# Optimization experiments

Hardware: AMD Instinct MI355X
Metric: run time of the kernel (lower is better)

## Reference

```python
import jax, jax.numpy as jnp
import numpy as np

DIM = 768
H = 12
DH = DIM // H          # 64
ROPE_DIM = (DH // 6) * 6   # 60
HALF = (ROPE_DIM // 3) // 2  # 10 freqs per axis
THETA = 10000.0
EPS = 1e-6


def rmsnorm(x, w):
    xf = x.astype(jnp.float32)
    var = jnp.mean(xf * xf, axis=-1, keepdims=True)
    return (w * (xf * jax.lax.rsqrt(var + EPS))).astype(x.dtype)


def rope_angles(positions):
    # positions: [B, N, 3] -> angles [B, N, 3*HALF]
    freqs = 1.0 / (THETA ** (jnp.arange(HALF, dtype=jnp.float32) / HALF))  # [HALF]
    # [B,N,3,1] * [1,1,1,HALF] -> [B,N,3,HALF] -> concat over axis order x,y,z
    ang = positions[..., :, None] * freqs[None, None, None, :]
    return ang.reshape(*positions.shape[:2], 3 * HALF)  # [B,N,30]


def apply_rope(t, cos, sin):
    # t: [B,N,H,ROPE_DIM]; cos/sin: [B,N,1,ROPE_DIM//2]
    B, N, Hh, D = t.shape
    tf = t.astype(jnp.float32).reshape(B, N, Hh, D // 2, 2)
    te, to = tf[..., 0], tf[..., 1]
    oe = te * cos - to * sin
    oo = te * sin + to * cos
    return jnp.stack([oe, oo], axis=-1).reshape(B, N, Hh, D).astype(t.dtype)


def setup_inputs() -> dict:
    key = jax.random.key(0)
    ks = jax.random.split(key, 5)
    B, N = 2, 2048
    x = jax.random.normal(ks[0], (B, N, DIM), dtype=jnp.float32)
    positions = jax.random.uniform(ks[1], (B, N, 3), dtype=jnp.float32)
    qkv_w = jax.random.normal(ks[2], (3 * DIM, DIM), dtype=jnp.float32) * (DIM ** -0.5)
    proj_w = jax.random.normal(ks[3], (DIM, DIM), dtype=jnp.float32) * (DIM ** -0.5)
    proj_b = jnp.zeros((DIM,), dtype=jnp.float32)
    qn_w = jnp.ones((DH,), dtype=jnp.float32)
    kn_w = jnp.ones((DH,), dtype=jnp.float32)
    return {"x": x, "positions": positions, "qkv_w": qkv_w, "proj_w": proj_w,
            "proj_b": proj_b, "qn_w": qn_w, "kn_w": kn_w}


def reference(x, positions, qkv_w, proj_w, proj_b, qn_w, kn_w):
    B, N, C = x.shape
    scale = DH ** -0.5
    qkv = (x @ qkv_w.T).reshape(B, N, 3, H, DH)
    q, k, v = qkv[:, :, 0], qkv[:, :, 1], qkv[:, :, 2]  # [B,N,H,DH]
    q = rmsnorm(q, qn_w)
    k = rmsnorm(k, kn_w)
    # 3D RoPE on first ROPE_DIM channels
    ang = rope_angles(positions)                 # [B,N,30]
    cos = jnp.cos(ang)[:, :, None, :]            # [B,N,1,30]
    sin = jnp.sin(ang)[:, :, None, :]
    q = jnp.concatenate([apply_rope(q[..., :ROPE_DIM], cos, sin), q[..., ROPE_DIM:]], axis=-1)
    k = jnp.concatenate([apply_rope(k[..., :ROPE_DIM], cos, sin), k[..., ROPE_DIM:]], axis=-1)
    attn = jnp.einsum('bqhd,bkhd->bhqk', q, k) * scale  # [B,H,N,N]
    attn = jax.nn.softmax(attn, axis=-1)
    out = jnp.einsum('bhqk,bkhd->bqhd', attn, v).reshape(B, N, C)
    return out @ proj_w.T + proj_b
```

## Files before the change

kernel.cpp:

```cpp
#include <hip/hip_runtime.h>
#include <hip/hip_bf16.h>
#include <math.h>

#define DIM 768
#define NH 12
#define DH 64
#define SEQ 2048
#define BATCH 2
#define TOK (BATCH*SEQ)
#define QKVN (3*DIM)

typedef __attribute__((ext_vector_type(8))) short bf16x8;
typedef __attribute__((ext_vector_type(4))) float f32x4;
typedef __attribute__((ext_vector_type(2))) unsigned int u32x2;
typedef unsigned short u16;

#define VM0 asm volatile("s_waitcnt vmcnt(0)" ::: "memory")
#define VM3 asm volatile("s_waitcnt vmcnt(3)" ::: "memory")
#define VM4 asm volatile("s_waitcnt vmcnt(4)" ::: "memory")
#define LGKM0 asm volatile("s_waitcnt lgkmcnt(0)" ::: "memory")
#define BAR() __builtin_amdgcn_s_barrier()

__device__ inline u16 f2bf(float f) {
  union { float f; unsigned u; } v; v.f = f;
  unsigned u = v.u;
  u += 0x7fffu + ((u >> 16) & 1u);
  return (u16)(u >> 16);
}

__device__ inline int pkbf(float a, float b) {
  __hip_bfloat162 h = __float22bfloat162_rn(make_float2(a, b));
  int r; __builtin_memcpy(&r, &h, 4); return r;
}

__global__ void conv_all(const float* __restrict__ a, u16* __restrict__ ao, int na4,
                         const float* __restrict__ b, u16* __restrict__ bo, int nb4,
                         const float* __restrict__ c, u16* __restrict__ co, int nc4,
                         const float* __restrict__ pos, float2* __restrict__ tab) {
  int i4 = blockIdx.x * blockDim.x + threadIdx.x;
  const int nconv = na4 + nb4 + nc4;
  if (i4 < nconv) {
    const float* src; u16* dst; int off;
    if (i4 < na4)            { src = a; dst = ao; off = i4; }
    else if (i4 < na4 + nb4) { src = b; dst = bo; off = i4 - na4; }
    else                     { src = c; dst = co; off = i4 - na4 - nb4; }
    float4 v = ((const float4*)src)[off];
    ushort4 o;
    o.x = f2bf(v.x); o.y = f2bf(v.y); o.z = f2bf(v.z); o.w = f2bf(v.w);
    ((ushort4*)dst)[off] = o;
    return;
  }
  int e = i4 - nconv;
  if (e >= TOK * 32) return;
  int t = e >> 5, p = e & 31;
  float cs = 1.f, sn = 0.f;
  if (p < 30) {
    int axis = p / 10, fi = p % 10;
    float freq = exp2f(-(float)fi * 1.3287712379549449f);
    float ang = pos[t * 3 + axis] * freq;
    cs = cosf(ang); sn = sinf(ang);
  }
  tab[e] = make_float2(cs, sn);
}

#define GLL(g, s) __builtin_amdgcn_global_load_lds((const __attribute__((address_space(1))) void*)(g), (__attribute__((address_space(3))) void*)(s), 16, 0, 0)

__global__ __launch_bounds__(256, 4) void gemm64(
    const u16* __restrict__ A, const u16* __restrict__ W,
    float* __restrict__ C, const float* __restrict__ bias,
    int M, int Nn, int K)
{
  __shared__ u16 As[2][64 * 64];
  __shared__ u16 Bs[2][64 * 64];
  const int t = threadIdx.x;
  const int w = t >> 6, l = t & 63;
  const int lr = l & 15, lg = l >> 4;
  const int wr = w >> 1, wc = w & 1;
  const int m0 = blockIdx.x * 64;
  const int n0 = blockIdx.y * 64;
  f32x4 acc[2][2] = {};
  const int srow = t >> 3;
  const int scol = (((t & 7) ^ (srow & 7)) * 8);
  const u16* aSrc = A + (size_t)(m0 + srow) * K + scol;
  const u16* bSrc = W + (size_t)(n0 + srow) * K + scol;
  const size_t r32 = (size_t)32 * K;
  const int sw = lr & 7;
  const int NT = K / 64;

  GLL(aSrc,       &As[0][w * 512]);
  GLL(aSrc + r32, &As[0][2048 + w * 512]);
  GLL(bSrc,       &Bs[0][w * 512]);
  GLL(bSrc + r32, &Bs[0][2048 + w * 512]);

  for (int kt = 0; kt < NT; ++kt) {
    const int cur = kt & 1;
    if (kt + 1 < NT) {
      const int k0 = (kt + 1) * 64;
      GLL(aSrc + k0,       &As[cur ^ 1][w * 512]);
      GLL(aSrc + r32 + k0, &As[cur ^ 1][2048 + w * 512]);
      GLL(bSrc + k0,       &Bs[cur ^ 1][w * 512]);
      GLL(bSrc + r32 + k0, &Bs[cur ^ 1][2048 + w * 512]);
      VM4;
    } else {
      VM0;
    }
    BAR();
#pragma unroll
    for (int kk = 0; kk < 2; ++kk) {
      bf16x8 af[2], bff[2];
#pragma unroll
      for (int mi = 0; mi < 2; ++mi)
        af[mi] = *(const bf16x8*)(&As[cur][0] + (wr * 32 + mi * 16 + lr) * 64 + (((kk * 4 + lg) ^ sw) * 8));
#pragma unroll
      for (int ni = 0; ni < 2; ++ni)
        bff[ni] = *(const bf16x8*)(&Bs[cur][0] + (wc * 32 + ni * 16 + lr) * 64 + (((kk * 4 + lg) ^ sw) * 8));
#pragma unroll
      for (int mi = 0; mi < 2; ++mi)
#pragma unroll
        for (int ni = 0; ni < 2; ++ni)
          acc[mi][ni] = __builtin_amdgcn_mfma_f32_16x16x32_bf16(af[mi], bff[ni], acc[mi][ni], 0, 0, 0);
    }
    LGKM0;
    BAR();
  }

#pragma unroll
  for (int mi = 0; mi < 2; ++mi)
#pragma unroll
    for (int ni = 0; ni < 2; ++ni)
#pragma unroll
      for (int r = 0; r < 4; ++r) {
        int row = m0 + wr * 32 + mi * 16 + lg * 4 + r;
        int col = n0 + wc * 32 + ni * 16 + lr;
        C[(size_t)row * Nn + col] = acc[mi][ni][r] + bias[col];
      }
}

__global__ __launch_bounds__(512, 6) void gemm_qkv(
    const u16* __restrict__ A, const u16* __restrict__ W,
    const float* __restrict__ qn_w, const float* __restrict__ kn_w,
    const float2* __restrict__ tab,
    u16* __restrict__ Qb, u16* __restrict__ Kb, u16* __restrict__ Vtb)
{
  __shared__ u16 As[2][128 * 64];
  __shared__ u16 Bs[2][64 * 64];
  const int K = DIM;
  const int t = threadIdx.x;
  const int w = t >> 6, l = t & 63;
  const int lr = l & 15, lg = l >> 4;
  const int m0 = blockIdx.x * 128;
  const int n0 = blockIdx.y * 64;
  f32x4 acc[4] = {};
  const int srow = t >> 3;
  const int scol = (((t & 7) ^ (srow & 7)) * 8);
  const u16* aSrc = A + (size_t)(m0 + srow) * K + scol;
  const u16* bSrc = W + (size_t)(n0 + srow) * K + scol;
  const size_t r64 = (size_t)64 * K;
  const int sw = lr & 7;
  const int NT = K / 64;

  GLL(aSrc,       &As[0][w * 512]);
  GLL(aSrc + r64, &As[0][4096 + w * 512]);
  GLL(bSrc,       &Bs[0][w * 512]);

  for (int kt = 0; kt < NT; ++kt) {
    const int cur = kt & 1;
    if (kt + 1 < NT) {
      const int k0 = (kt + 1) * 64;
      GLL(aSrc + k0,       &As[cur ^ 1][w * 512]);
      GLL(aSrc + r64 + k0, &As[cur ^ 1][4096 + w * 512]);
      GLL(bSrc + k0,       &Bs[cur ^ 1][w * 512]);
      VM3;
    } else {
      VM0;
    }
    BAR();
#pragma unroll
    for (int kk = 0; kk < 2; ++kk) {
      bf16x8 af = *(const bf16x8*)(&As[cur][0] + (w * 16 + lr) * 64 + (((kk * 4 + lg) ^ sw) * 8));
      bf16x8 bff[4];
#pragma unroll
      for (int ni = 0; ni < 4; ++ni)
        bff[ni] = *(const bf16x8*)(&Bs[cur][0] + (ni * 16 + lr) * 64 + (((kk * 4 + lg) ^ sw) * 8));
#pragma unroll
      for (int ni = 0; ni < 4; ++ni)
        acc[ni] = __builtin_amdgcn_mfma_f32_16x16x32_bf16(af, bff[ni], acc[ni], 0, 0, 0);
    }
    LGKM0;
    BAR();
  }

  const int chunk = n0 >> 6;
  const int tt = chunk / 12;
  const int h  = chunk % 12;
  const int bB = m0 >> 11;
  const int bh = bB * NH + h;

  if (tt == 2) {
    const int nbase = (m0 + w * 16 + lg * 4) & 2047;
#pragma unroll
    for (int ni = 0; ni < 4; ++ni) {
      const int d = ni * 16 + lr;
      ushort4 o;
      o.x = f2bf(acc[ni][0]); o.y = f2bf(acc[ni][1]);
      o.z = f2bf(acc[ni][2]); o.w = f2bf(acc[ni][3]);
      *(ushort4*)(Vtb + ((size_t)bh * DH + d) * SEQ + nbase) = o;
    }
  } else {
    const float* wv = (tt == 0 ? qn_w : kn_w);
    const float qs = (tt == 0 ? 0.125f * 1.4426950408889634f : 1.f);
    float wgt[4];
#pragma unroll
    for (int ni = 0; ni < 4; ++ni) wgt[ni] = wv[ni * 16 + lr];
    u16* outp = (tt == 0 ? Qb : Kb) + (size_t)bh * SEQ * DH;
#pragma unroll
    for (int r = 0; r < 4; ++r) {
      float ss = 0.f;
#pragma unroll
      for (int ni = 0; ni < 4; ++ni) ss += acc[ni][r] * acc[ni][r];
      ss += __shfl_xor(ss, 1, 64);
      ss += __shfl_xor(ss, 2, 64);
      ss += __shfl_xor(ss, 4, 64);
      ss += __shfl_xor(ss, 8, 64);
      const float rms = rsqrtf(ss * (1.f / 64.f) + 1e-6f);
      const int trow = m0 + w * 16 + lg * 4 + r;
      const float2* tl = tab + trow * 32;
      u16* rowp = outp + (size_t)(trow & 2047) * DH;
#pragma unroll
      for (int ni = 0; ni < 4; ++ni) {
        const int d = ni * 16 + lr;
        float v = acc[ni][r] * rms * wgt[ni];
        float vp = __shfl_xor(v, 1, 64);
        float2 cssn = tl[ni * 8 + (lr >> 1)];
        float sgn = (d & 1) ? cssn.y : -cssn.y;
        rowp[d] = f2bf((v * cssn.x + vp * sgn) * qs);
      }
    }
  }
}

__global__ __launch_bounds__(256, 3) void attn(
    const u16* __restrict__ Qb, const u16* __restrict__ Kb,
    const u16* __restrict__ Vtb, u16* __restrict__ Ob)
{
  __shared__ u16 Ks[2][2][64 * 64];
  __shared__ u16 Vs[2][64 * 64];
  const int tid = threadIdx.x;
  const int w = tid >> 6, l = tid & 63;
  const int lr = l & 15, lg = l >> 4;
  const int qg = w & 1, half = w >> 1;
  const int wg = blockIdx.x;
  const int swz = (wg & 7) * 96 + (wg >> 3);
  const int bh = swz >> 5;
  const int q0 = (swz & 31) * 64;
  const u16* Qp = Qb + (size_t)bh * SEQ * DH;
  const u16* Kp = Kb + (size_t)bh * SEQ * DH;
  const u16* Vp = Vtb + (size_t)bh * DH * SEQ;

  const int qrA = q0 + qg * 32 + lr;
  const bf16x8 bq0a = *(const bf16x8*)(Qp + (size_t)qrA * DH + 8 * lg);
  const bf16x8 bq1a = *(const bf16x8*)(Qp + (size_t)qrA * DH + 32 + 8 * lg);
  const bf16x8 bq0b = *(const bf16x8*)(Qp + (size_t)(qrA + 16) * DH + 8 * lg);
  const bf16x8 bq1b = *(const bf16x8*)(Qp + (size_t)(qrA + 16) * DH + 32 + 8 * lg);

  const int srow = tid >> 3;
  const int sc16 = (tid & 7) ^ (srow & 7);
  const u16* kSrc = Kp + (size_t)srow * DH + sc16 * 8;
  const u16* vSrc = Vp + (size_t)srow * SEQ + sc16 * 8;

  const int frow = (lr & 3) | ((lr & 4) << 1) | ((lr & 8) >> 1);
  const int ksw = frow & 7;
  const int vsw = lr & 7;

  bf16x8 vone;
#pragma unroll
  for (int j = 0; j < 8; ++j) vone[j] = (short)0x3F80;

  f32x4 oaccA[4] = {}, oaccB[4] = {};
  f32x4 laccA = {}, laccB = {};

  GLL(kSrc,          &Ks[0][0][w * 512]);
  GLL(kSrc + 2048,   &Ks[0][0][w * 512 + 2048]);
  GLL(kSrc + 4096,   &Ks[0][1][w * 512]);
  GLL(kSrc + 6144,   &Ks[0][1][w * 512 + 2048]);
  VM0;
  BAR();
  GLL(vSrc,              &Vs[0][w * 512]);
  GLL(vSrc + 65536,      &Vs[0][w * 512 + 2048]);
  GLL(vSrc + 64,         &Vs[1][w * 512]);
  GLL(vSrc + 64 + 65536, &Vs[1][w * 512 + 2048]);
  GLL(kSrc + 8192,   &Ks[1][0][w * 512]);
  GLL(kSrc + 10240,  &Ks[1][0][w * 512 + 2048]);
  GLL(kSrc + 12288,  &Ks[1][1][w * 512]);
  GLL(kSrc + 14336,  &Ks[1][1][w * 512 + 2048]);

  for (int i = 0; i < 16; ++i) {
    const int p = i & 1;
    const u16* Kt = &Ks[p][half][0];
    const u16* Vt = &Vs[half][0];

    f32x4 paccA[4] = {}, paccB[4] = {};
    __builtin_amdgcn_s_setprio(1);
#pragma unroll
    for (int c = 0; c < 4; ++c) {
      const int rbase = (16 * c + frow) * 64;
      bf16x8 ka = *(const bf16x8*)(Kt + rbase + ((lg ^ ksw) * 8));
      bf16x8 kb = *(const bf16x8*)(Kt + rbase + (((4 + lg) ^ ksw) * 8));
      paccA[c] = __builtin_amdgcn_mfma_f32_16x16x32_bf16(ka, bq0a, paccA[c], 0, 0, 0);
      paccA[c] = __builtin_amdgcn_mfma_f32_16x16x32_bf16(kb, bq1a, paccA[c], 0, 0, 0);
      paccB[c] = __builtin_amdgcn_mfma_f32_16x16x32_bf16(ka, bq0b, paccB[c], 0, 0, 0);
      paccB[c] = __builtin_amdgcn_mfma_f32_16x16x32_bf16(kb, bq1b, paccB[c], 0, 0, 0);
    }
    __builtin_amdgcn_s_setprio(0);

    union { unsigned d[4]; bf16x8 v; } puA[2], puB[2];
#pragma unroll
    for (int g = 0; g < 2; ++g) {
      const int clo = 2 * g, chi = 2 * g + 1;
      float eA[8], eB[8];
#pragma unroll
      for (int r = 0; r < 4; ++r) {
        eA[r]     = __builtin_amdgcn_exp2f(paccA[clo][r] - 12.f);
        eA[4 + r] = __builtin_amdgcn_exp2f(paccA[chi][r] - 12.f);
        eB[r]     = __builtin_amdgcn_exp2f(paccB[clo][r] - 12.f);
        eB[4 + r] = __builtin_amdgcn_exp2f(paccB[chi][r] - 12.f);
      }
      u32x2 a0 = __builtin_amdgcn_permlane32_swap((unsigned)pkbf(eA[0], eA[1]),
                                                  (unsigned)pkbf(eA[4], eA[5]), false, false);
      u32x2 a1 = __builtin_amdgcn_permlane32_swap((unsigned)pkbf(eA[2], eA[3]),
                                                  (unsigned)pkbf(eA[6], eA[7]), false, false);
      u32x2 b0 = __builtin_amdgcn_permlane32_swap((unsigned)pkbf(eB[0], eB[1]),
                                                  (unsigned)pkbf(eB[4], eB[5]), false, false);
      u32x2 b1 = __builtin_amdgcn_permlane32_swap((unsigned)pkbf(eB[2], eB[3]),
                                                  (unsigned)pkbf(eB[6], eB[7]), false, false);
      puA[g].d[0] = a0[0]; puA[g].d[1] = a1[0]; puA[g].d[2] = a0[1]; puA[g].d[3] = a1[1];
      puB[g].d[0] = b0[0]; puB[g].d[1] = b1[0]; puB[g].d[2] = b0[1]; puB[g].d[3] = b1[1];
    }

    if (i < 15) { VM4; } else { VM0; }
    BAR();

    __builtin_amdgcn_s_setprio(1);
#pragma unroll
    for (int g = 0; g < 2; ++g) {
#pragma unroll
      for (int dt = 0; dt < 4; ++dt) {
        bf16x8 va = *(const bf16x8*)(Vt + (16 * dt + lr) * 64 + (((4 * g + lg) ^ vsw) * 8));
        oaccA[dt] = __builtin_amdgcn_mfma_f32_16x16x32_bf16(va, puA[g].v, oaccA[dt], 0, 0, 0);
        oaccB[dt] = __builtin_amdgcn_mfma_f32_16x16x32_bf16(va, puB[g].v, oaccB[dt], 0, 0, 0);
      }
      laccA = __builtin_amdgcn_mfma_f32_16x16x32_bf16(vone, puA[g].v, laccA, 0, 0, 0);
      laccB = __builtin_amdgcn_mfma_f32_16x16x32_bf16(vone, puB[g].v, laccB, 0, 0, 0);
    }
    __builtin_amdgcn_s_setprio(0);

    LGKM0;
    VM0;
    BAR();

    if (i + 1 < 16) {
      const size_t vo = (size_t)(2 * i + 2) * 64;
      GLL(vSrc + vo,              &Vs[0][w * 512]);
      GLL(vSrc + vo + 65536,      &Vs[0][w * 512 + 2048]);
      GLL(vSrc + vo + 64,         &Vs[1][w * 512]);
      GLL(vSrc + vo + 64 + 65536, &Vs[1][w * 512 + 2048]);
    }
    if (i + 2 < 16) {
      const size_t ko = (size_t)(2 * i + 4) * 4096;
      GLL(kSrc + ko,        &Ks[p][0][w * 512]);
      GLL(kSrc + ko + 2048, &Ks[p][0][w * 512 + 2048]);
      GLL(kSrc + ko + 4096, &Ks[p][1][w * 512]);
      GLL(kSrc + ko + 6144, &Ks[p][1][w * 512 + 2048]);
    }
  }

  float* scr = (float*)&Ks[0][0][0];
  const int sidA = (qg * 2 + 0) * 64 + l;
  const int sidB = (qg * 2 + 1) * 64 + l;
  if (half == 1) {
#pragma unroll
    for (int dt = 0; dt < 4; ++dt)
#pragma unroll
      for (int r = 0; r < 4; ++r) {
        scr[sidA * 17 + dt * 4 + r] = oaccA[dt][r];
        scr[sidB * 17 + dt * 4 + r] = oaccB[dt][r];
      }
    scr[sidA * 17 + 16] = laccA[0];
    scr[sidB * 17 + 16] = laccB[0];
  }
  __syncthreads();
  if (half == 1) return;
#pragma unroll
  for (int dt = 0; dt < 4; ++dt)
#pragma unroll
    for (int r = 0; r < 4; ++r) {
      oaccA[dt][r] += scr[sidA * 17 + dt * 4 + r];
      oaccB[dt][r] += scr[sidB * 17 + dt * 4 + r];
    }
  const float invA = 1.f / (laccA[0] + scr[sidA * 17 + 16]);
  const float invB = 1.f / (laccB[0] + scr[sidB * 17 + 16]);

  const int b = bh / NH, h = bh % NH;
  const int qA = q0 + qg * 32 + lr;
  size_t obA = (size_t)(b * SEQ + qA) * DIM + h * DH + 4 * lg;
  size_t obB = (size_t)(b * SEQ + qA + 16) * DIM + h * DH + 4 * lg;
#pragma unroll
  for (int dt = 0; dt < 4; ++dt) {
    ushort4 oA, oB;
    oA.x = f2bf(oaccA[dt][0] * invA); oA.y = f2bf(oaccA[dt][1] * invA);
    oA.z = f2bf(oaccA[dt][2] * invA); oA.w = f2bf(oaccA[dt][3] * invA);
    oB.x = f2bf(oaccB[dt][0] * invB); oB.y = f2bf(oaccB[dt][1] * invB);
    oB.z = f2bf(oaccB[dt][2] * invB); oB.w = f2bf(oaccB[dt][3] * invB);
    *(ushort4*)(Ob + obA + 16 * dt) = oA;
    *(ushort4*)(Ob + obB + 16 * dt) = oB;
  }
}

extern "C" void kernel_launch(void* const* d_in, const int* in_sizes, int n_in,
                              void* d_out, int out_size, void* d_ws, size_t ws_size,
                              hipStream_t stream) {
  const float* x      = (const float*)d_in[0];
  const float* pos    = (const float*)d_in[1];
  const float* qkv_w  = (const float*)d_in[2];
  const float* proj_w = (const float*)d_in[3];
  const float* proj_b = (const float*)d_in[4];
  const float* qn_w   = (const float*)d_in[5];
  const float* kn_w   = (const float*)d_in[6];
  char* ws = (char*)d_ws;
  u16*    xb    = (u16*)(ws + 0);
  u16*    wqkv  = (u16*)(ws + 6291456);
  u16*    wproj = (u16*)(ws + 9830400);
  float2* tab   = (float2*)(ws + 11010048);
  u16*    Qb    = (u16*)(ws + 12058624);
  u16*    Kb    = (u16*)(ws + 18350080);
  u16*    Vtb   = (u16*)(ws + 24641536);
  u16*    Ob    = (u16*)(ws + 30932992);
  float* out = (float*)d_out;

  const int na4 = TOK * DIM / 4, nb4 = QKVN * DIM / 4, nc4 = DIM * DIM / 4;
  const int ntot = na4 + nb4 + nc4 + TOK * 32;
  conv_all<<<(ntot + 255) / 256, 256, 0, stream>>>(
      x, xb, na4, qkv_w, wqkv, nb4, proj_w, wproj, nc4, pos, tab);

  dim3 g1(TOK / 128, QKVN / 64);
  gemm_qkv<<<g1, 512, 0, stream>>>(xb, wqkv, qn_w, kn_w, tab, Qb, Kb, Vtb);

  attn<<<SEQ / 64 * BATCH * NH, 256, 0, stream>>>(Qb, Kb, Vtb, Ob);

  dim3 g3(TOK / 64, DIM / 64);
  gemm64<<<g3, 256, 0, stream>>>(Ob, wproj, out, proj_b, TOK, DIM, DIM);
}
```

Measured before the change: 88.62 us.

## Load V tiles straight into registers and restructure K prefetch pipeline

The attention kernel stops staging V through shared memory. Each wave now issues global_load_dwordx4 directly into registers in the MFMA operand layout, prefetching the next tile while the current one is consumed. K is double-buffered in LDS with a one-tile-ahead prefetch, and one barrier plus a full vmcnt(0) drain per iteration are removed, replaced with finer vmcnt waits and a scheduling barrier. This reduces LDS traffic, LDS footprint and synchronisation. The cost is strided, less coalesced global reads for V, more live registers, and the hand-counted waitcnt ordering must stay correct.

```diff
diff --git a/kernel.cpp b/kernel.cpp
--- a/kernel.cpp
+++ b/kernel.cpp
@@ -18,8 +18,10 @@
 #define VM0 asm volatile("s_waitcnt vmcnt(0)" ::: "memory")
 #define VM3 asm volatile("s_waitcnt vmcnt(3)" ::: "memory")
 #define VM4 asm volatile("s_waitcnt vmcnt(4)" ::: "memory")
+#define VM8 asm volatile("s_waitcnt vmcnt(8)" ::: "memory")
 #define LGKM0 asm volatile("s_waitcnt lgkmcnt(0)" ::: "memory")
 #define BAR() __builtin_amdgcn_s_barrier()
+#define SCHED0 __builtin_amdgcn_sched_barrier(0)
 
 __device__ inline u16 f2bf(float f) {
   union { float f; unsigned u; } v; v.f = f;
@@ -31,6 +33,18 @@
 __device__ inline int pkbf(float a, float b) {
   __hip_bfloat162 h = __float22bfloat162_rn(make_float2(a, b));
   int r; __builtin_memcpy(&r, &h, 4); return r;
+}
+
+template<int OFF>
+__device__ inline bf16x8 gl16(const u16* base, unsigned voff) {
+  bf16x8 r;
+  if constexpr (OFF)
+    asm volatile("global_load_dwordx4 %0, %1, %2 offset:64"
+                 : "=&v"(r) : "v"(voff), "s"(base) : "memory");
+  else
+    asm volatile("global_load_dwordx4 %0, %1, %2"
+                 : "=&v"(r) : "v"(voff), "s"(base) : "memory");
+  return r;
 }
 
 __global__ void conv_all(const float* __restrict__ a, u16* __restrict__ ao, int na4,
@@ -244,7 +258,6 @@
     const u16* __restrict__ Vtb, u16* __restrict__ Ob)
 {
   __shared__ u16 Ks[2][2][64 * 64];
-  __shared__ u16 Vs[2][64 * 64];
   const int tid = threadIdx.x;
   const int w = tid >> 6, l = tid & 63;
   const int lr = l & 15, lg = l >> 4;
@@ -266,11 +279,14 @@
   const int srow = tid >> 3;
   const int sc16 = (tid & 7) ^ (srow & 7);
   const u16* kSrc = Kp + (size_t)srow * DH + sc16 * 8;
-  const u16* vSrc = Vp + (size_t)srow * SEQ + sc16 * 8;
 
   const int frow = (lr & 3) | ((lr & 4) << 1) | ((lr & 8) >> 1);
   const int ksw = frow & 7;
-  const int vsw = lr & 7;
+
+  unsigned vvo[4];
+#pragma unroll
+  for (int dt = 0; dt < 4; ++dt)
+    vvo[dt] = (unsigned)(((16 * dt + lr) * SEQ + 8 * lg + 64 * half) * 2);
 
   bf16x8 vone;
 #pragma unroll
@@ -278,26 +294,29 @@
 
   f32x4 oaccA[4] = {}, oaccB[4] = {};
   f32x4 laccA = {}, laccB = {};
-
-  GLL(kSrc,          &Ks[0][0][w * 512]);
-  GLL(kSrc + 2048,   &Ks[0][0][w * 512 + 2048]);
-  GLL(kSrc + 4096,   &Ks[0][1][w * 512]);
-  GLL(kSrc + 6144,   &Ks[0][1][w * 512 + 2048]);
+  bf16x8 vva[4], vvb[4];
+
+  GLL(kSrc,        &Ks[0][0][w * 512]);
+  GLL(kSrc + 2048, &Ks[0][0][w * 512 + 2048]);
+  GLL(kSrc + 4096, &Ks[0][1][w * 512]);
+  GLL(kSrc + 6144, &Ks[0][1][w * 512 + 2048]);
   VM0;
   BAR();
-  GLL(vSrc,              &Vs[0][w * 512]);
-  GLL(vSrc + 65536,      &Vs[0][w * 512 + 2048]);
-  GLL(vSrc + 64,         &Vs[1][w * 512]);
-  GLL(vSrc + 64 + 65536, &Vs[1][w * 512 + 2048]);
-  GLL(kSrc + 8192,   &Ks[1][0][w * 512]);
-  GLL(kSrc + 10240,  &Ks[1][0][w * 512 + 2048]);
-  GLL(kSrc + 12288,  &Ks[1][1][w * 512]);
-  GLL(kSrc + 14336,  &Ks[1][1][w * 512 + 2048]);
+#pragma unroll
+  for (int dt = 0; dt < 4; ++dt) vva[dt] = gl16<0>(Vp, vvo[dt]);
+#pragma unroll
+  for (int dt = 0; dt < 4; ++dt) vvb[dt] = gl16<1>(Vp, vvo[dt]);
 
   for (int i = 0; i < 16; ++i) {
     const int p = i & 1;
+    if (i + 1 < 16) {
+      const u16* kb_ = kSrc + (size_t)(i + 1) * 8192;
+      GLL(kb_,        &Ks[p ^ 1][0][w * 512]);
+      GLL(kb_ + 2048, &Ks[p ^ 1][0][w * 512 + 2048]);
+      GLL(kb_ + 4096, &Ks[p ^ 1][1][w * 512]);
+      GLL(kb_ + 6144, &Ks[p ^ 1][1][w * 512 + 2048]);
+    }
     const u16* Kt = &Ks[p][half][0];
-    const u16* Vt = &Vs[half][0];
 
     f32x4 paccA[4] = {}, paccB[4] = {};
     __builtin_amdgcn_s_setprio(1);
@@ -337,15 +356,15 @@
       puB[g].d[0] = b0[0]; puB[g].d[1] = b1[0]; puB[g].d[2] = b0[1]; puB[g].d[3] = b1[1];
     }
 
-    if (i < 15) { VM4; } else { VM0; }
-    BAR();
+    if (i + 1 < 16) { VM4; } else { VM0; }
+    SCHED0;
 
     __builtin_amdgcn_s_setprio(1);
 #pragma unroll
     for (int g = 0; g < 2; ++g) {
 #pragma unroll
       for (int dt = 0; dt < 4; ++dt) {
-        bf16x8 va = *(const bf16x8*)(Vt + (16 * dt + lr) * 64 + (((4 * g + lg) ^ vsw) * 8));
+        bf16x8 va = g ? vvb[dt] : vva[dt];
         oaccA[dt] = __builtin_amdgcn_mfma_f32_16x16x32_bf16(va, puA[g].v, oaccA[dt], 0, 0, 0);
         oaccB[dt] = __builtin_amdgcn_mfma_f32_16x16x32_bf16(va, puB[g].v, oaccB[dt], 0, 0, 0);
       }
@@ -354,26 +373,20 @@
     }
     __builtin_amdgcn_s_setprio(0);
 
-    LGKM0;
-    VM0;
-    BAR();
-
     if (i + 1 < 16) {
-      const size_t vo = (size_t)(2 * i + 2) * 64;
-      GLL(vSrc + vo,              &Vs[0][w * 512]);
-      GLL(vSrc + vo + 65536,      &Vs[0][w * 512 + 2048]);
-      GLL(vSrc + vo + 64,         &Vs[1][w * 512]);
-      GLL(vSrc + vo + 64 + 65536, &Vs[1][w * 512 + 2048]);
-    }
-    if (i + 2 < 16) {
-      const size_t ko = (size_t)(2 * i + 4) * 4096;
-      GLL(kSrc + ko,        &Ks[p][0][w * 512]);
-      GLL(kSrc + ko + 2048, &Ks[p][0][w * 512 + 2048]);
-      GLL(kSrc + ko + 4096, &Ks[p][1][w * 512]);
-      GLL(kSrc + ko + 6144, &Ks[p][1][w * 512 + 2048]);
-    }
-  }
-
+      const u16* vb_ = Vp + (size_t)(i + 1) * 128;
+#pragma unroll
+      for (int dt = 0; dt < 4; ++dt) vva[dt] = gl16<0>(vb_, vvo[dt]);
+#pragma unroll
+      for (int dt = 0; dt < 4; ++dt) vvb[dt] = gl16<1>(vb_, vvo[dt]);
+      LGKM0;
+      VM8;
+      BAR();
+    }
+  }
+
+  LGKM0;
+  __syncthreads();
   float* scr = (float*)&Ks[0][0][0];
   const int sidA = (qg * 2 + 0) * 64 + l;
   const int sidB = (qg * 2 + 1) * 64 + l;
```

New measurement: 103.0 us. 1.16x slower.
